# Kernel tuning notes

Measured on AMD Instinct MI355X. Metric: run time of the kernel, lower is better.

Reference implementation:

```python
import jax, jax.numpy as jnp
import numpy as np

B = 64
RX, RZ, RX_, RZ_ = 32, 16, 16, 8
TN = 1
STRIDE = 2
IN_DIM, OUT_DIM = 256, 512
KEY_DIM, H, ATTN_RATIO = 32, 8, 2
D = ATTN_RATIO * KEY_DIM            # per-head value dim = 64
DH = D * H                          # 512
NH_KD = KEY_DIM * H                 # 256
N = RX * RX + TN * RZ * RZ          # 1280 tokens (search + template)
N_ = RX_ * RX_ + TN * RZ_ * RZ_     # 320 subsampled query tokens
SCALE = KEY_DIM ** -0.5
EPS = 1e-5


def linear_bn(x, W, gamma, beta):
    # Linear (no bias) followed by BatchNorm1d in training mode over (B*N, C)
    y = jnp.einsum('bnc,oc->bno', x, W)
    m = y.mean(axis=(0, 1))
    v = y.var(axis=(0, 1))  # biased variance, as torch BN uses for normalization
    return (y - m) * jax.lax.rsqrt(v + EPS) * gamma + beta


def subsample(x):
    # stride-subsample the search-region tokens and each template's tokens
    b, n, c = x.shape
    parts = [x[:, :RX * RX].reshape(b, RX, RX, c)[:, ::STRIDE, ::STRIDE].reshape(b, -1, c)]
    for i in range(TN):
        s = RX * RX + i * RZ * RZ
        z = x[:, s:s + RZ * RZ].reshape(b, RZ, RZ, c)[:, ::STRIDE, ::STRIDE].reshape(b, -1, c)
        parts.append(z)
    return jnp.concatenate(parts, axis=1)


def setup_inputs() -> dict:
    key = jax.random.key(0)
    ks = jax.random.split(key, 4)
    return {
        'x': jax.random.normal(ks[0], (B, N, IN_DIM), dtype=jnp.float32),
        'W_kv': jax.random.normal(ks[1], (NH_KD + DH, IN_DIM), dtype=jnp.float32) * 0.02,
        'g_kv': jnp.ones((NH_KD + DH,), jnp.float32),
        'b_kv': jnp.zeros((NH_KD + DH,), jnp.float32),
        'W_q': jax.random.normal(ks[2], (NH_KD, IN_DIM), dtype=jnp.float32) * 0.02,
        'g_q': jnp.ones((NH_KD,), jnp.float32),
        'b_q': jnp.zeros((NH_KD,), jnp.float32),
        'W_p': jax.random.normal(ks[3], (OUT_DIM, DH), dtype=jnp.float32) * 0.02,
        'g_p': jnp.ones((OUT_DIM,), jnp.float32),
        'b_p': jnp.zeros((OUT_DIM,), jnp.float32),
    }


def reference(x, W_kv, g_kv, b_kv, W_q, g_q, b_q, W_p, g_p, b_p):
    b = x.shape[0]
    # fused KV projection + BN, then split into per-head K and V
    kv = linear_bn(x, W_kv, g_kv, b_kv).reshape(b, N, H, KEY_DIM + D)
    k = kv[..., :KEY_DIM].transpose(0, 2, 1, 3)   # [B,H,N,key_dim]
    v = kv[..., KEY_DIM:].transpose(0, 2, 1, 3)   # [B,H,N,d]
    # Q: subsample tokens, then Linear_BN
    q = linear_bn(subsample(x), W_q, g_q, b_q).reshape(b, N_, H, KEY_DIM).transpose(0, 2, 1, 3)
    attn = jax.nn.softmax(jnp.einsum('bhqd,bhkd->bhqk', q, k) * SCALE, axis=-1)
    o = jnp.einsum('bhqk,bhkd->bhqd', attn, v).transpose(0, 2, 1, 3).reshape(b, N_, DH)
    return linear_bn(jax.nn.hard_swish(o), W_p, g_p, b_p)
```

## Files before the change

### kernel.cpp

```cpp
#include <hip/hip_runtime.h>
#include <hip/hip_bf16.h>
#include <math.h>

#define EPSF 1e-5f
#define SCALEF 0.17677669529663687f
#define LOG2E 1.4426950408889634f

typedef unsigned short u16;
typedef unsigned int u32;
typedef __attribute__((ext_vector_type(8))) short bf16x8;
typedef __attribute__((ext_vector_type(4))) float f32x4;

__device__ __forceinline__ float b2f(u16 u) {
    union { unsigned int i; float f; } v; v.i = ((unsigned int)u) << 16; return v.f;
}
__device__ __forceinline__ u16 f2b(float f) {
    union { float f; unsigned int i; } v; v.f = f;
    unsigned int x = v.i;
    return (u16)((x + 0x7fffu + ((x >> 16) & 1u)) >> 16);
}
__device__ __forceinline__ float fexp2(float x) {
#if __has_builtin(__builtin_amdgcn_exp2f)
    return __builtin_amdgcn_exp2f(x);
#else
    return exp2f(x);
#endif
}
__device__ __forceinline__ u32 cvtpk_bf16(float lo, float hi) {
    u32 r;
    asm("v_cvt_pk_bf16_f32 %0, %1, %2" : "=v"(r) : "v"(lo), "v"(hi));
    return r;
}

__global__ void convert_f32_bf16(const float* __restrict__ src, u16* __restrict__ dst, int n4) {
    int i = blockIdx.x * 256 + threadIdx.x;
    if (i >= n4) return;
    float4 v = ((const float4*)src)[i];
    ushort4 o;
    o.x = f2b(v.x); o.y = f2b(v.y); o.z = f2b(v.z); o.w = f2b(v.w);
    ((ushort4*)dst)[i] = o;
}

__global__ void gather_sub_bf16(const u16* __restrict__ xb, u16* __restrict__ xsub, int n8) {
    int i = blockIdx.x * 256 + threadIdx.x;
    if (i >= n8) return;
    int e = i << 3;
    int row = e >> 8;
    int col = e & 255;
    int b = row / 320;
    int t = row - b * 320;
    int n;
    if (t < 256) n = ((t >> 4) << 6) + ((t & 15) << 1);
    else { int tt = t - 256; n = 1024 + ((tt >> 3) << 5) + ((tt & 7) << 1); }
    *(int4*)(xsub + e) = *(const int4*)(xb + ((size_t)(b * 1280 + n)) * 256 + col);
}

template<int OUT_F32>
__global__ __launch_bounds__(256) void gemm_bt(const u16* __restrict__ A, const u16* __restrict__ Bw,
                                               void* __restrict__ Cv, int M, int N, int K,
                                               float* __restrict__ sums) {
    __shared__ u16 As[128 * 40];
    __shared__ u16 Bs[128 * 40];
    __shared__ float sumbuf[4][64][2];
    const int tid = threadIdx.x;
    const int wave = tid >> 6, lane = tid & 63;
    const int quad = lane >> 4, lc = lane & 15;
    const int wr = wave >> 1, wc = wave & 1;
    const int m0 = blockIdx.x * 128, n0 = blockIdx.y * 128;
    const int lrow = tid >> 2;
    const int lk = (tid & 3) << 3;

    f32x4 acc[4][4];
#pragma unroll
    for (int i = 0; i < 4; ++i)
#pragma unroll
        for (int j = 0; j < 4; ++j) acc[i][j] = (f32x4){0.f, 0.f, 0.f, 0.f};

    for (int k0 = 0; k0 < K; k0 += 32) {
        __syncthreads();
        *(int4*)&As[lrow * 40 + lk]        = *(const int4*)(A  + (size_t)(m0 + lrow) * K + k0 + lk);
        *(int4*)&As[(lrow + 64) * 40 + lk] = *(const int4*)(A  + (size_t)(m0 + lrow + 64) * K + k0 + lk);
        *(int4*)&Bs[lrow * 40 + lk]        = *(const int4*)(Bw + (size_t)(n0 + lrow) * K + k0 + lk);
        *(int4*)&Bs[(lrow + 64) * 40 + lk] = *(const int4*)(Bw + (size_t)(n0 + lrow + 64) * K + k0 + lk);
        __syncthreads();
        bf16x8 af[4], bfr[4];
#pragma unroll
        for (int mi = 0; mi < 4; ++mi) af[mi]  = *(const bf16x8*)&As[(wr * 64 + mi * 16 + lc) * 40 + quad * 8];
#pragma unroll
        for (int ni = 0; ni < 4; ++ni) bfr[ni] = *(const bf16x8*)&Bs[(wc * 64 + ni * 16 + lc) * 40 + quad * 8];
#pragma unroll
        for (int mi = 0; mi < 4; ++mi)
#pragma unroll
            for (int ni = 0; ni < 4; ++ni)
                acc[mi][ni] = __builtin_amdgcn_mfma_f32_16x16x32_bf16(af[mi], bfr[ni], acc[mi][ni], 0, 0, 0);
    }
    float ps[4], ps2[4];
#pragma unroll
    for (int ni = 0; ni < 4; ++ni) { ps[ni] = 0.f; ps2[ni] = 0.f; }
#pragma unroll
    for (int mi = 0; mi < 4; ++mi)
#pragma unroll
        for (int ni = 0; ni < 4; ++ni)
#pragma unroll
            for (int r = 0; r < 4; ++r) {
                int row = m0 + wr * 64 + mi * 16 + quad * 4 + r;
                int cn  = n0 + wc * 64 + ni * 16 + lc;
                float v = acc[mi][ni][r];
                ps[ni] += v; ps2[ni] += v * v;
                if (OUT_F32) ((float*)Cv)[(size_t)row * N + cn] = v;
                else         ((u16*)Cv)[(size_t)row * N + cn] = f2b(v);
            }
#pragma unroll
    for (int ni = 0; ni < 4; ++ni) {
        ps[ni]  += __shfl_xor(ps[ni], 16);  ps[ni]  += __shfl_xor(ps[ni], 32);
        ps2[ni] += __shfl_xor(ps2[ni], 16); ps2[ni] += __shfl_xor(ps2[ni], 32);
    }
    if (quad == 0) {
#pragma unroll
        for (int ni = 0; ni < 4; ++ni) {
            sumbuf[wave][ni * 16 + lc][0] = ps[ni];
            sumbuf[wave][ni * 16 + lc][1] = ps2[ni];
        }
    }
    __syncthreads();
    {
        int which = tid & 1, idx = (tid >> 1) & 63, wcg = tid >> 7;
        int channel = n0 + wcg * 64 + idx;
        float v = sumbuf[wcg][idx][which] + sumbuf[wcg + 2][idx][which];
        int rep = blockIdx.x & 7;
        atomicAdd(&sums[(rep * 2 + which) * N + channel], v);
    }
}

__global__ void finalize_bn(const float* __restrict__ sum2, const float* __restrict__ g,
                            const float* __restrict__ beta, int cols, float inv_n, float scale,
                            float* __restrict__ AB) {
    int c = blockIdx.x * 256 + threadIdx.x;
    if (c >= cols) return;
    float s = 0.f, s2 = 0.f;
#pragma unroll
    for (int r = 0; r < 8; ++r) {
        s  += sum2[(r * 2 + 0) * cols + c];
        s2 += sum2[(r * 2 + 1) * cols + c];
    }
    float m = s * inv_n;
    float var = s2 * inv_n - m * m;
    float a = g[c] * rsqrtf(var + EPSF) * scale;
    AB[c] = a;
    AB[cols + c] = beta[c] * scale - m * a;
}

__global__ __launch_bounds__(256) void normalize_kv(const u16* __restrict__ kv, const float* __restrict__ AB,
                                                    u16* __restrict__ Kn, u16* __restrict__ Vtn) {
    __shared__ u16 Vs[64 * 66];
    const int h = blockIdx.x, nt = blockIdx.y, b = blockIdx.z;
    const int bh = b * 8 + h;
    const int tid = threadIdx.x;
    {
        int tok = tid >> 2, dk = (tid & 3) << 3;
        size_t src = ((size_t)(b * 1280 + nt * 64 + tok)) * 768 + h * 96 + dk;
        union { int4 v; u16 u[8]; } ld; ld.v = *(const int4*)(kv + src);
        union { int4 v; u16 u[8]; } st;
#pragma unroll
        for (int j = 0; j < 8; ++j) {
            int c = h * 96 + dk + j;
            st.u[j] = f2b(b2f(ld.u[j]) * AB[c] + AB[768 + c]);
        }
        int g = tok >> 5, kk = tok & 31;
        int rowp = nt * 64 + g * 32 + ((kk & 4) << 2) + ((kk >> 3) << 2) + (kk & 3);
        *(int4*)(Kn + ((size_t)bh * 1280 + rowp) * 32 + dk) = st.v;
    }
#pragma unroll
    for (int half = 0; half < 2; ++half) {
        int t = (tid >> 3) + half * 32;
        int dv = (tid & 7) << 3;
        size_t src = ((size_t)(b * 1280 + nt * 64 + t)) * 768 + h * 96 + 32 + dv;
        union { int4 v; u16 u[8]; } ld; ld.v = *(const int4*)(kv + src);
#pragma unroll
        for (int j = 0; j < 8; ++j) {
            int c = h * 96 + 32 + dv + j;
            Vs[(dv + j) * 66 + t] = f2b(b2f(ld.u[j]) * AB[c] + AB[768 + c]);
        }
    }
    __syncthreads();
#pragma unroll
    for (int half = 0; half < 2; ++half) {
        int d = (tid >> 3) + half * 32;
        int tc = (tid & 7) << 3;
        union { int4 v; u16 u[8]; } st;
#pragma unroll
        for (int j = 0; j < 8; ++j) st.u[j] = Vs[d * 66 + tc + j];
        *(int4*)(Vtn + ((size_t)bh * 64 + d) * 1280 + nt * 64 + tc) = st.v;
    }
}

__global__ __launch_bounds__(256, 2) void attn_kernel4(const u16* __restrict__ Kn, const u16* __restrict__ Vtn,
                                                       const u16* __restrict__ q_raw, const float* __restrict__ ABq,
                                                       u16* __restrict__ o_act) {
    const int tid = threadIdx.x;
    const int wave = tid >> 6, lane = tid & 63;
    const int quad = lane >> 4, lc = lane & 15;
    const int h = blockIdx.x, b = blockIdx.y;
    const int bh = b * 8 + h;

    float qa[8], qb[8];
#pragma unroll
    for (int j = 0; j < 8; ++j) { int c = h * 32 + quad * 8 + j; qa[j] = ABq[c]; qb[j] = ABq[256 + c]; }
    bf16x8 qf[5];
#pragma unroll
    for (int j = 0; j < 5; ++j) {
        const u16* qs = q_raw + ((size_t)(b * 320 + j * 64 + wave * 16 + lc)) * 256 + h * 32 + quad * 8;
        union { int4 v; u16 u[8]; } ld; ld.v = *(const int4*)qs;
        union { bf16x8 v; u16 u[8]; } st;
#pragma unroll
        for (int jj = 0; jj < 8; ++jj) st.u[jj] = f2b(b2f(ld.u[jj]) * qa[jj] + qb[jj]);
        qf[j] = st.v;
    }

    const u16* Kp = Kn + (size_t)bh * 1280 * 32 + lc * 32 + quad * 8;
    const u16* Vp = Vtn + (size_t)bh * 64 * 1280 + lc * 1280 + quad * 8;

    f32x4 acc[5][4];
#pragma unroll
    for (int j = 0; j < 5; ++j)
#pragma unroll
        for (int i = 0; i < 4; ++i) acc[j][i] = (f32x4){0.f, 0.f, 0.f, 0.f};
    float lsum[5];
#pragma unroll
    for (int j = 0; j < 5; ++j) lsum[j] = 0.f;

    const f32x4 z = (f32x4){0.f, 0.f, 0.f, 0.f};
    for (int kc = 0; kc < 1280; kc += 32) {
        bf16x8 kfA = *(const bf16x8*)(Kp + kc * 32);
        bf16x8 kfB = *(const bf16x8*)(Kp + kc * 32 + 512);
        bf16x8 vf0 = *(const bf16x8*)(Vp + kc);
        bf16x8 vf1 = *(const bf16x8*)(Vp + 16 * 1280 + kc);
        bf16x8 vf2 = *(const bf16x8*)(Vp + 32 * 1280 + kc);
        bf16x8 vf3 = *(const bf16x8*)(Vp + 48 * 1280 + kc);
        f32x4 s0[5], s1[5];
#pragma unroll
        for (int j = 0; j < 5; ++j) {
            s0[j] = __builtin_amdgcn_mfma_f32_16x16x32_bf16(kfA, qf[j], z, 0, 0, 0);
            s1[j] = __builtin_amdgcn_mfma_f32_16x16x32_bf16(kfB, qf[j], z, 0, 0, 0);
        }
#pragma unroll
        for (int j = 0; j < 5; ++j) {
            float p0 = fexp2(s0[j][0]);
            float p1 = fexp2(s0[j][1]);
            float p2 = fexp2(s0[j][2]);
            float p3 = fexp2(s0[j][3]);
            float p4 = fexp2(s1[j][0]);
            float p5 = fexp2(s1[j][1]);
            float p6 = fexp2(s1[j][2]);
            float p7 = fexp2(s1[j][3]);
            lsum[j] += ((p0 + p1) + (p2 + p3)) + ((p4 + p5) + (p6 + p7));
            union { u32 w[4]; bf16x8 v; } pf;
            pf.w[0] = cvtpk_bf16(p0, p1);
            pf.w[1] = cvtpk_bf16(p2, p3);
            pf.w[2] = cvtpk_bf16(p4, p5);
            pf.w[3] = cvtpk_bf16(p6, p7);
            acc[j][0] = __builtin_amdgcn_mfma_f32_16x16x32_bf16(vf0, pf.v, acc[j][0], 0, 0, 0);
            acc[j][1] = __builtin_amdgcn_mfma_f32_16x16x32_bf16(vf1, pf.v, acc[j][1], 0, 0, 0);
            acc[j][2] = __builtin_amdgcn_mfma_f32_16x16x32_bf16(vf2, pf.v, acc[j][2], 0, 0, 0);
            acc[j][3] = __builtin_amdgcn_mfma_f32_16x16x32_bf16(vf3, pf.v, acc[j][3], 0, 0, 0);
        }
    }
#pragma unroll
    for (int j = 0; j < 5; ++j) {
        float l = lsum[j];
        l += __shfl_xor(l, 16);
        l += __shfl_xor(l, 32);
        float inv = 1.f / l;
        int qrow = b * 320 + j * 64 + wave * 16 + lc;
        u16* dst = o_act + (size_t)qrow * 512 + h * 64 + quad * 4;
#pragma unroll
        for (int nt = 0; nt < 4; ++nt) {
            ushort4 st;
#pragma unroll
            for (int r = 0; r < 4; ++r) {
                float o = acc[j][nt][r] * inv;
                float hs = o * fminf(fmaxf(o + 3.f, 0.f), 6.f) * (1.f / 6.f);
                ((u16*)&st)[r] = f2b(hs);
            }
            *(ushort4*)(dst + nt * 16) = st;
        }
    }
}

__global__ void bn_apply_out(const float* __restrict__ praw, const float* __restrict__ ABp,
                             float* __restrict__ out, int n4) {
    int i = blockIdx.x * 256 + threadIdx.x;
    if (i >= n4) return;
    int e = i << 2;
    int c = e & 511;
    float4 v = ((const float4*)praw)[i];
    float4 o;
    o.x = v.x * ABp[c]     + ABp[512 + c];
    o.y = v.y * ABp[c + 1] + ABp[512 + c + 1];
    o.z = v.z * ABp[c + 2] + ABp[512 + c + 2];
    o.w = v.w * ABp[c + 3] + ABp[512 + c + 3];
    ((float4*)out)[i] = o;
}

extern "C" void kernel_launch(void* const* d_in, const int* in_sizes, int n_in,
                              void* d_out, int out_size, void* d_ws, size_t ws_size,
                              hipStream_t stream) {
    const float* x   = (const float*)d_in[0];
    const float* Wkv = (const float*)d_in[1];
    const float* gkv = (const float*)d_in[2];
    const float* bkv = (const float*)d_in[3];
    const float* Wq  = (const float*)d_in[4];
    const float* gq  = (const float*)d_in[5];
    const float* bq  = (const float*)d_in[6];
    const float* Wp  = (const float*)d_in[7];
    const float* gp  = (const float*)d_in[8];
    const float* bp  = (const float*)d_in[9];
    float* out = (float*)d_out;

    char* ws = (char*)d_ws;
    size_t off = 0;
    auto alloc = [&](size_t bytes) -> void* {
        void* p = ws + off;
        off += (bytes + 255) & ~(size_t)255;
        return p;
    };
    u16*   kv_raw = (u16*)alloc(81920ull * 768 * 2);
    u16*   q_raw  = (u16*)alloc(20480ull * 256 * 2);
    void*  slot1  = alloc(81920ull * 256 * 2);
    u16*   x_b    = (u16*)slot1;
    u16*   K_norm = (u16*)slot1;
    float* p_raw  = (float*)slot1;
    void*  slot2  = alloc(20480ull * 512 * 2);
    u16*   xsub_b = (u16*)slot2;
    u16*   o_act  = (u16*)slot2;
    u16*   Vt_norm = (u16*)alloc(512ull * 64 * 1280 * 2);
    u16*   Wkv_b  = (u16*)alloc(768ull * 256 * 2);
    u16*   Wq_b   = (u16*)alloc(256ull * 256 * 2);
    u16*   Wp_b   = (u16*)alloc(512ull * 512 * 2);
    float* sums_kv = (float*)alloc(8 * 2 * 768 * sizeof(float));
    float* sums_q  = (float*)alloc(8 * 2 * 256 * sizeof(float));
    float* sums_p  = (float*)alloc(8 * 2 * 512 * sizeof(float));
    float* ABkv = (float*)alloc(1536 * sizeof(float));
    float* ABq  = (float*)alloc(512 * sizeof(float));
    float* ABp  = (float*)alloc(1024 * sizeof(float));

    dim3 blk(256);
    hipMemsetAsync(sums_kv, 0, 8 * 2 * (768 + 256 + 512) * sizeof(float), stream);

    convert_f32_bf16<<<20480, blk, 0, stream>>>(x,   x_b,   5242880);
    convert_f32_bf16<<<192,   blk, 0, stream>>>(Wkv, Wkv_b, 49152);
    convert_f32_bf16<<<64,    blk, 0, stream>>>(Wq,  Wq_b,  16384);
    convert_f32_bf16<<<256,   blk, 0, stream>>>(Wp,  Wp_b,  65536);
    gather_sub_bf16<<<2560,   blk, 0, stream>>>(x_b, xsub_b, 655360);

    gemm_bt<0><<<dim3(640, 6), blk, 0, stream>>>(x_b, Wkv_b, kv_raw, 81920, 768, 256, sums_kv);
    gemm_bt<0><<<dim3(160, 2), blk, 0, stream>>>(xsub_b, Wq_b, q_raw, 20480, 256, 256, sums_q);

    finalize_bn<<<3, blk, 0, stream>>>(sums_kv, gkv, bkv, 768, 1.f / 81920.f, 1.f, ABkv);
    finalize_bn<<<1, blk, 0, stream>>>(sums_q,  gq,  bq,  256, 1.f / 20480.f, SCALEF * LOG2E, ABq);

    normalize_kv<<<dim3(8, 20, 64), blk, 0, stream>>>(kv_raw, ABkv, K_norm, Vt_norm);

    attn_kernel4<<<dim3(8, 64), blk, 0, stream>>>(K_norm, Vt_norm, q_raw, ABq, o_act);

    gemm_bt<1><<<dim3(160, 4), blk, 0, stream>>>(o_act, Wp_b, p_raw, 20480, 512, 512, sums_p);
    finalize_bn<<<2, blk, 0, stream>>>(sums_p, gp, bp, 512, 1.f / 20480.f, 1.f, ABp);

    bn_apply_out<<<10240, blk, 0, stream>>>(p_raw, ABp, out, 2621440);
}
```

Before: 398.7 us.

## Use direct global-to-LDS loads in GEMM and swap grid order for weight reuse

The GEMM tile loads now use global_load_lds, which moves data straight from global memory into LDS without passing through registers, and the padded LDS stride of 40 becomes an unpadded 32. The grid dimensions are swapped so that consecutive blocks share the same A row-tile across N tiles, which should improve L2 reuse of the activations. The unpadded layout may bring back LDS bank conflicts on the fragment reads, and the explicit vmcnt(0) wait keeps the loop unpipelined.

```diff
diff --git a/kernel.cpp b/kernel.cpp
--- a/kernel.cpp
+++ b/kernel.cpp
@@ -30,6 +30,11 @@
     u32 r;
     asm("v_cvt_pk_bf16_f32 %0, %1, %2" : "=v"(r) : "v"(lo), "v"(hi));
     return r;
+}
+__device__ __forceinline__ void gload_lds16(const u16* __restrict__ g, u16* l) {
+    __builtin_amdgcn_global_load_lds(
+        (const __attribute__((address_space(1))) void*)g,
+        (__attribute__((address_space(3))) void*)l, 16, 0, 0);
 }
 
 __global__ void convert_f32_bf16(const float* __restrict__ src, u16* __restrict__ dst, int n4) {
@@ -59,16 +64,25 @@
 __global__ __launch_bounds__(256) void gemm_bt(const u16* __restrict__ A, const u16* __restrict__ Bw,
                                                void* __restrict__ Cv, int M, int N, int K,
                                                float* __restrict__ sums) {
-    __shared__ u16 As[128 * 40];
-    __shared__ u16 Bs[128 * 40];
+    __shared__ u16 As[128 * 32];
+    __shared__ u16 Bs[128 * 32];
     __shared__ float sumbuf[4][64][2];
     const int tid = threadIdx.x;
     const int wave = tid >> 6, lane = tid & 63;
     const int quad = lane >> 4, lc = lane & 15;
     const int wr = wave >> 1, wc = wave & 1;
-    const int m0 = blockIdx.x * 128, n0 = blockIdx.y * 128;
-    const int lrow = tid >> 2;
-    const int lk = (tid & 3) << 3;
+    const int m0 = blockIdx.y * 128, n0 = blockIdx.x * 128;
+
+    const int srow = (wave << 5) + (lane >> 2);
+    const int scol = (lane & 3) << 3;
+    u16* ldsA0 = As + ((wave << 5) + 0) * 32;
+    u16* ldsA1 = As + ((wave << 5) + 16) * 32;
+    u16* ldsB0 = Bs + ((wave << 5) + 0) * 32;
+    u16* ldsB1 = Bs + ((wave << 5) + 16) * 32;
+    const u16* gA0 = A  + (size_t)(m0 + srow) * K + scol;
+    const u16* gA1 = A  + (size_t)(m0 + srow + 16) * K + scol;
+    const u16* gB0 = Bw + (size_t)(n0 + srow) * K + scol;
+    const u16* gB1 = Bw + (size_t)(n0 + srow + 16) * K + scol;
 
     f32x4 acc[4][4];
 #pragma unroll
@@ -78,16 +92,17 @@
 
     for (int k0 = 0; k0 < K; k0 += 32) {
         __syncthreads();
-        *(int4*)&As[lrow * 40 + lk]        = *(const int4*)(A  + (size_t)(m0 + lrow) * K + k0 + lk);
-        *(int4*)&As[(lrow + 64) * 40 + lk] = *(const int4*)(A  + (size_t)(m0 + lrow + 64) * K + k0 + lk);
-        *(int4*)&Bs[lrow * 40 + lk]        = *(const int4*)(Bw + (size_t)(n0 + lrow) * K + k0 + lk);
-        *(int4*)&Bs[(lrow + 64) * 40 + lk] = *(const int4*)(Bw + (size_t)(n0 + lrow + 64) * K + k0 + lk);
+        gload_lds16(gA0 + k0, ldsA0);
+        gload_lds16(gA1 + k0, ldsA1);
+        gload_lds16(gB0 + k0, ldsB0);
+        gload_lds16(gB1 + k0, ldsB1);
+        asm volatile("s_waitcnt vmcnt(0)" ::: "memory");
         __syncthreads();
         bf16x8 af[4], bfr[4];
 #pragma unroll
-        for (int mi = 0; mi < 4; ++mi) af[mi]  = *(const bf16x8*)&As[(wr * 64 + mi * 16 + lc) * 40 + quad * 8];
-#pragma unroll
-        for (int ni = 0; ni < 4; ++ni) bfr[ni] = *(const bf16x8*)&Bs[(wc * 64 + ni * 16 + lc) * 40 + quad * 8];
+        for (int mi = 0; mi < 4; ++mi) af[mi]  = *(const bf16x8*)&As[(wr * 64 + mi * 16 + lc) * 32 + quad * 8];
+#pragma unroll
+        for (int ni = 0; ni < 4; ++ni) bfr[ni] = *(const bf16x8*)&Bs[(wc * 64 + ni * 16 + lc) * 32 + quad * 8];
 #pragma unroll
         for (int mi = 0; mi < 4; ++mi)
 #pragma unroll
@@ -127,7 +142,7 @@
         int which = tid & 1, idx = (tid >> 1) & 63, wcg = tid >> 7;
         int channel = n0 + wcg * 64 + idx;
         float v = sumbuf[wcg][idx][which] + sumbuf[wcg + 2][idx][which];
-        int rep = blockIdx.x & 7;
+        int rep = blockIdx.y & 7;
         atomicAdd(&sums[(rep * 2 + which) * N + channel], v);
     }
 }
@@ -353,8 +368,8 @@
     convert_f32_bf16<<<256,   blk, 0, stream>>>(Wp,  Wp_b,  65536);
     gather_sub_bf16<<<2560,   blk, 0, stream>>>(x_b, xsub_b, 655360);
 
-    gemm_bt<0><<<dim3(640, 6), blk, 0, stream>>>(x_b, Wkv_b, kv_raw, 81920, 768, 256, sums_kv);
-    gemm_bt<0><<<dim3(160, 2), blk, 0, stream>>>(xsub_b, Wq_b, q_raw, 20480, 256, 256, sums_q);
+    gemm_bt<0><<<dim3(6, 640), blk, 0, stream>>>(x_b, Wkv_b, kv_raw, 81920, 768, 256, sums_kv);
+    gemm_bt<0><<<dim3(2, 160), blk, 0, stream>>>(xsub_b, Wq_b, q_raw, 20480, 256, 256, sums_q);
 
     finalize_bn<<<3, blk, 0, stream>>>(sums_kv, gkv, bkv, 768, 1.f / 81920.f, 1.f, ABkv);
     finalize_bn<<<1, blk, 0, stream>>>(sums_q,  gq,  bq,  256, 1.f / 20480.f, SCALEF * LOG2E, ABq);
@@ -363,7 +378,7 @@
 
     attn_kernel4<<<dim3(8, 64), blk, 0, stream>>>(K_norm, Vt_norm, q_raw, ABq, o_act);
 
-    gemm_bt<1><<<dim3(160, 4), blk, 0, stream>>>(o_act, Wp_b, p_raw, 20480, 512, 512, sums_p);
+    gemm_bt<1><<<dim3(4, 160), blk, 0, stream>>>(o_act, Wp_b, p_raw, 20480, 512, 512, sums_p);
     finalize_bn<<<2, blk, 0, stream>>>(sums_p, gp, bp, 512, 1.f / 20480.f, 1.f, ABp);
 
     bn_apply_out<<<10240, blk, 0, stream>>>(p_raw, ABp, out, 2621440);
```

Result: no change. 398.1 us (-0.1%).
